# Performance work log

Hardware: AMD Instinct MI355X
Metric: run time of the kernel (lower is better)

Reference implementation:

```python
import jax, jax.numpy as jnp
import numpy as np

N_NODES = 50000
N_REL = 16
D_EMB = 128
D_HID = 128
D_OUT = 128
N_EDGES = 1600000


def _xavier(key, shape, fan_in, fan_out, dtype=jnp.float32):
    lim = float(np.sqrt(6.0 / (fan_in + fan_out)))
    return jax.random.uniform(key, shape, dtype, -lim, lim)


def setup_inputs() -> dict:
    key = jax.random.key(0)
    ks = jax.random.split(key, 10)
    edge_index = jax.random.randint(ks[0], (2, N_EDGES), 0, N_NODES, dtype=jnp.int64)
    edge_type = jax.random.randint(ks[1], (N_EDGES,), 0, N_REL, dtype=jnp.int64)
    emb = _xavier(ks[2], (N_NODES, D_EMB), N_NODES, D_EMB)
    W1 = _xavier(ks[3], (N_REL, D_EMB, D_HID), D_EMB, D_HID)
    root1 = _xavier(ks[4], (D_EMB, D_HID), D_EMB, D_HID)
    b1 = jnp.zeros((D_HID,), jnp.float32)
    W2 = _xavier(ks[5], (N_REL, D_HID, D_OUT), D_HID, D_OUT)
    root2 = _xavier(ks[6], (D_HID, D_OUT), D_HID, D_OUT)
    b2 = jnp.zeros((D_OUT,), jnp.float32)
    return {"edge_index": edge_index, "edge_type": edge_type, "emb": emb,
            "W1": W1, "root1": root1, "b1": b1,
            "W2": W2, "root2": root2, "b2": b2}


def rgcn_conv(x, edge_index, edge_type, W, W_root, b):
    """PyG RGCNConv (num_bases=None): out_i = x_i @ W_root + b + sum_r mean_{j in N_r(i)} x_j @ W_r.
    Mean-aggregate x_j per (dst, relation) first, then apply relation GEMMs (linearity)."""
    src, dst = edge_index[0], edge_index[1]
    seg = dst * N_REL + edge_type                      # [E] composite (node, rel) key
    x_src = x[src]                                     # [E, d] gather
    summed = jax.ops.segment_sum(x_src, seg, num_segments=N_NODES * N_REL)  # [N*R, d]
    cnt = jax.ops.segment_sum(jnp.ones((src.shape[0],), x.dtype), seg,
                              num_segments=N_NODES * N_REL)                 # [N*R]
    agg = summed / jnp.maximum(cnt, 1.0)[:, None]      # mean; empty (i,r) -> 0
    agg = agg.reshape(N_NODES, N_REL, x.shape[1])      # [N, R, d]
    return jnp.einsum('nrd,rdh->nh', agg, W) + x @ W_root + b


def reference(edge_index, edge_type, emb, W1, root1, b1, W2, root2, b2):
    x = emb                                            # embedding.weight: all-node lookup
    x = jax.nn.relu(rgcn_conv(x, edge_index, edge_type, W1, root1, b1))
    # dropout(p=0.5) omitted: eval-mode identity
    x = rgcn_conv(x, edge_index, edge_type, W2, root2, b2)
    return x
```

## Files before the change

kernel.cpp:

```cpp
#include <hip/hip_runtime.h>

#define N_NODES 50000
#define N_REL 16
#define D 128
#define N_SEG (N_NODES * N_REL)
#define N_SEG4 (N_SEG / 4)

typedef short bf16x8 __attribute__((ext_vector_type(8)));
typedef float f32x4 __attribute__((ext_vector_type(4)));
typedef unsigned short u16;
typedef unsigned int u32;

__device__ __forceinline__ u16 f32_to_bf16(float f) {
  u32 u = __builtin_bit_cast(u32, f);
  u32 r = (u + 0x7FFFu + ((u >> 16) & 1u)) >> 16;
  return (u16)r;
}
__device__ __forceinline__ float bf16_to_f32(u16 h) {
  u32 u = ((u32)h) << 16;
  return __builtin_bit_cast(float, u);
}

__global__ __launch_bounds__(256) void k_count(const int* __restrict__ dst,
                                               const int* __restrict__ rel,
                                               int* __restrict__ cnt, int E) {
  int e = (blockIdx.x * blockDim.x + threadIdx.x) * 2;
  if (e < E)     atomicAdd(&cnt[dst[e] * N_REL + rel[e]], 1);
  if (e + 1 < E) atomicAdd(&cnt[dst[e + 1] * N_REL + rel[e + 1]], 1);
}

__global__ __launch_bounds__(256) void k_bsum2(const int4* __restrict__ cnt4,
                                               int* __restrict__ bsum, int n4) {
  __shared__ int sm[256];
  int idx = blockIdx.x * 256 + threadIdx.x;
  int v = 0;
  if (idx < n4) { int4 c = cnt4[idx]; v = c.x + c.y + c.z + c.w; }
  sm[threadIdx.x] = v;
  __syncthreads();
  for (int s = 128; s > 0; s >>= 1) {
    if (threadIdx.x < s) sm[threadIdx.x] += sm[threadIdx.x + s];
    __syncthreads();
  }
  if (threadIdx.x == 0) bsum[blockIdx.x] = sm[0];
}

__global__ __launch_bounds__(1024) void k_bscan2(int* __restrict__ bsum, int nb) {
  __shared__ int sm[1024];
  int i = threadIdx.x;
  int v = (i < nb) ? bsum[i] : 0;
  sm[i] = v;
  __syncthreads();
  for (int s = 1; s < 1024; s <<= 1) {
    int t = (i >= s) ? sm[i - s] : 0;
    __syncthreads();
    sm[i] += t;
    __syncthreads();
  }
  if (i < nb) bsum[i] = sm[i] - v;
}

__global__ __launch_bounds__(256) void k_off2(const int4* __restrict__ cnt4,
                                              const int* __restrict__ bsum,
                                              int* __restrict__ off, int n4) {
  __shared__ int sm[256];
  int idx = blockIdx.x * 256 + threadIdx.x;
  int4 c = {0, 0, 0, 0};
  if (idx < n4) c = cnt4[idx];
  int tsum = c.x + c.y + c.z + c.w;
  sm[threadIdx.x] = tsum;
  __syncthreads();
  for (int s = 1; s < 256; s <<= 1) {
    int t = (threadIdx.x >= s) ? sm[threadIdx.x - s] : 0;
    __syncthreads();
    sm[threadIdx.x] += t;
    __syncthreads();
  }
  int base = bsum[blockIdx.x] + sm[threadIdx.x] - tsum;
  if (idx < n4) {
    int4 o;
    o.x = base;
    o.y = base + c.x;
    o.z = o.y + c.y;
    o.w = o.z + c.z;
    ((int4*)off)[idx] = o;
    if (idx == n4 - 1) off[4 * n4] = o.w + c.w;
  }
}

__global__ __launch_bounds__(256) void k_fill(const int* __restrict__ src,
                                              const int* __restrict__ dst,
                                              const int* __restrict__ rel,
                                              const int* __restrict__ off,
                                              int* __restrict__ cnt,
                                              int* __restrict__ bucket, int E) {
  int e = (blockIdx.x * blockDim.x + threadIdx.x) * 2;
  if (e < E) {
    int seg = dst[e] * N_REL + rel[e];
    int old = atomicSub(&cnt[seg], 1);
    bucket[off[seg] + old - 1] = src[e];
  }
  if (e + 1 < E) {
    int seg = dst[e + 1] * N_REL + rel[e + 1];
    int old = atomicSub(&cnt[seg], 1);
    bucket[off[seg] + old - 1] = src[e + 1];
  }
}

__device__ __forceinline__ void wfrag_one(const float* __restrict__ W,
                                          u16* __restrict__ Wf, int tid) {
  int lane = tid & 63;
  int t = (tid >> 6) & 7;
  int kb = tid >> 9;
  int h = t * 16 + (lane & 15);
  int kbase = kb * 32 + ((lane >> 4) << 3);
  bf16x8 frag;
#pragma unroll
  for (int j = 0; j < 8; ++j) {
    int k = kbase + j;
    frag[j] = (short)f32_to_bf16(W[(size_t)(k >> 7) * (D * D) + (size_t)(k & 127) * D + h]);
  }
  *(bf16x8*)(Wf + (size_t)tid * 8) = frag;
}

#define ZERO_U4 N_SEG4
#define CVT_N4 (N_NODES * D / 4)
#define WF_T (64 * 8 * 64)
#define RF_T (4 * 8 * 64)
#define PREP_TOTAL (ZERO_U4 + CVT_N4 + 2 * WF_T + 2 * RF_T)

__global__ __launch_bounds__(256) void k_prep(int* __restrict__ cnt,
                                              const float* __restrict__ emb,
                                              u16* __restrict__ embb,
                                              const float* __restrict__ W1,
                                              u16* __restrict__ Wf1,
                                              const float* __restrict__ W2,
                                              u16* __restrict__ Wf2,
                                              const float* __restrict__ R1,
                                              u16* __restrict__ Rf1,
                                              const float* __restrict__ R2,
                                              u16* __restrict__ Rf2) {
  int tid = blockIdx.x * blockDim.x + threadIdx.x;
  if (tid < ZERO_U4) {
    uint4 z; z.x = z.y = z.z = z.w = 0u;
    ((uint4*)cnt)[tid] = z;
    return;
  }
  int u = tid - ZERO_U4;
  if (u < CVT_N4) {
    float4 v = ((const float4*)emb)[u];
    u32 p0 = (u32)f32_to_bf16(v.x) | ((u32)f32_to_bf16(v.y) << 16);
    u32 p1 = (u32)f32_to_bf16(v.z) | ((u32)f32_to_bf16(v.w) << 16);
    ((u32*)embb)[u * 2] = p0;
    ((u32*)embb)[u * 2 + 1] = p1;
    return;
  }
  u -= CVT_N4;
  if (u < WF_T) { wfrag_one(W1, Wf1, u); return; }
  u -= WF_T;
  if (u < WF_T) { wfrag_one(W2, Wf2, u); return; }
  u -= WF_T;
  if (u < RF_T) { wfrag_one(R1, Rf1, u); return; }
  u -= RF_T;
  if (u < RF_T) { wfrag_one(R2, Rf2, u); return; }
}

template <int L>
__global__ __launch_bounds__(256) void k_layer(const int* __restrict__ off,
                                               const int* __restrict__ bucket,
                                               const u16* __restrict__ x,
                                               const u16* __restrict__ Wf,
                                               const u16* __restrict__ Rf,
                                               const float* __restrict__ bias,
                                               u16* __restrict__ outb,
                                               float* __restrict__ outf) {
  __shared__ f32x4 red[4][4][64];
  int w = threadIdx.x >> 6;
  int lane = threadIdx.x & 63;
  int node0 = blockIdx.x << 4;
  int m = lane & 15;
  int q = lane >> 4;
  int node = node0 + m;

  f32x4 acc[8];
#pragma unroll
  for (int t = 0; t < 8; ++t)
#pragma unroll
    for (int i = 0; i < 4; ++i) acc[t][i] = 0.0f;

  {
    bf16x8 a = *(const bf16x8*)(x + ((size_t)node << 7) + w * 32 + (q << 3));
    const u16* bp = Rf + ((size_t)w << 12) + ((size_t)lane << 3);
#pragma unroll
    for (int t = 0; t < 8; ++t) {
      bf16x8 b = *(const bf16x8*)(bp + t * 512);
      acc[t] = __builtin_amdgcn_mfma_f32_16x16x32_bf16(a, b, acc[t], 0, 0, 0);
    }
  }

  for (int rr = 0; rr < 4; ++rr) {
    int r = (w << 2) + rr;
    int seg = (node << 4) + r;
    int o0 = off[seg];
    int o1 = off[seg + 1];

    float a0[8], a1[8], a2[8], a3[8];
#pragma unroll
    for (int j = 0; j < 8; ++j) { a0[j] = 0.f; a1[j] = 0.f; a2[j] = 0.f; a3[j] = 0.f; }

    int i = o0;
    int s = (i < o1) ? bucket[i] : 0;
    while (i < o1) {
      const u16* xs = x + ((size_t)s << 7) + (q << 3);
      bf16x8 v0 = *(const bf16x8*)(xs);
      bf16x8 v1 = *(const bf16x8*)(xs + 32);
      bf16x8 v2 = *(const bf16x8*)(xs + 64);
      bf16x8 v3 = *(const bf16x8*)(xs + 96);
      int snext = (i + 1 < o1) ? bucket[i + 1] : 0;
#pragma unroll
      for (int j = 0; j < 8; ++j) {
        a0[j] += bf16_to_f32((u16)v0[j]);
        a1[j] += bf16_to_f32((u16)v1[j]);
        a2[j] += bf16_to_f32((u16)v2[j]);
        a3[j] += bf16_to_f32((u16)v3[j]);
      }
      s = snext;
      ++i;
    }

    float sc = (o1 > o0) ? 1.0f / (float)(o1 - o0) : 0.0f;
    bf16x8 f0, f1, f2, f3;
#pragma unroll
    for (int j = 0; j < 8; ++j) {
      f0[j] = (short)f32_to_bf16(a0[j] * sc);
      f1[j] = (short)f32_to_bf16(a1[j] * sc);
      f2[j] = (short)f32_to_bf16(a2[j] * sc);
      f3[j] = (short)f32_to_bf16(a3[j] * sc);
    }

    const u16* bp = Wf + ((size_t)(r * 4) << 12) + ((size_t)lane << 3);
#pragma unroll
    for (int t = 0; t < 8; ++t) {
      bf16x8 b0 = *(const bf16x8*)(bp + t * 512);
      bf16x8 b1 = *(const bf16x8*)(bp + 4096 + t * 512);
      bf16x8 b2 = *(const bf16x8*)(bp + 8192 + t * 512);
      bf16x8 b3 = *(const bf16x8*)(bp + 12288 + t * 512);
      acc[t] = __builtin_amdgcn_mfma_f32_16x16x32_bf16(f0, b0, acc[t], 0, 0, 0);
      acc[t] = __builtin_amdgcn_mfma_f32_16x16x32_bf16(f1, b1, acc[t], 0, 0, 0);
      acc[t] = __builtin_amdgcn_mfma_f32_16x16x32_bf16(f2, b2, acc[t], 0, 0, 0);
      acc[t] = __builtin_amdgcn_mfma_f32_16x16x32_bf16(f3, b3, acc[t], 0, 0, 0);
    }
  }

#pragma unroll
  for (int half = 0; half < 2; ++half) {
#pragma unroll
    for (int t = 0; t < 4; ++t) red[w][t][lane] = acc[half * 4 + t];
    __syncthreads();
    {
      f32x4 s0 = red[0][w][lane];
      f32x4 s1 = red[1][w][lane];
      f32x4 s2 = red[2][w][lane];
      f32x4 s3 = red[3][w][lane];
      int tt = half * 4 + w;
      int h = tt * 16 + m;
      float bv = bias[h];
#pragma unroll
      for (int r4 = 0; r4 < 4; ++r4) {
        int n = node0 + (q << 2) + r4;
        float v = s0[r4] + s1[r4] + s2[r4] + s3[r4] + bv;
        if (L == 1) {
          v = v > 0.0f ? v : 0.0f;
          outb[(size_t)n * D + h] = f32_to_bf16(v);
        } else {
          outf[(size_t)n * D + h] = v;
        }
      }
    }
    if (half == 0) __syncthreads();
  }
}

extern "C" void kernel_launch(void* const* d_in, const int* in_sizes, int n_in,
                              void* d_out, int out_size, void* d_ws, size_t ws_size,
                              hipStream_t stream) {
  const int* edge_index = (const int*)d_in[0];
  const int* edge_type  = (const int*)d_in[1];
  const float* emb   = (const float*)d_in[2];
  const float* W1    = (const float*)d_in[3];
  const float* root1 = (const float*)d_in[4];
  const float* b1    = (const float*)d_in[5];
  const float* W2    = (const float*)d_in[6];
  const float* root2 = (const float*)d_in[7];
  const float* b2    = (const float*)d_in[8];
  float* out = (float*)d_out;

  int E = in_sizes[0] / 2;
  const int* src = edge_index;
  const int* dst = edge_index + E;
  int scanBlocks = (N_SEG4 + 255) / 256;

  char* ws = (char*)d_ws;
  size_t off_b = 0;
  auto take = [&](size_t bytes) -> char* {
    char* p = ws + off_b;
    off_b += (bytes + 255) & ~(size_t)255;
    return p;
  };
  int*   cnt    = (int*)take((size_t)N_SEG * 4);
  int*   offs   = (int*)take((size_t)(N_SEG + 1) * 4);
  int*   bsum   = (int*)take((size_t)scanBlocks * 4);
  int*   bucket = (int*)take((size_t)E * 4);
  u16*   embb   = (u16*)take((size_t)N_NODES * D * 2);
  u16*   x1     = (u16*)take((size_t)N_NODES * D * 2);
  u16*   Wf1    = (u16*)take((size_t)64 * 8 * 512 * 2);
  u16*   Rf1    = (u16*)take((size_t)4 * 8 * 512 * 2);
  u16*   Wf2    = (u16*)take((size_t)64 * 8 * 512 * 2);
  u16*   Rf2    = (u16*)take((size_t)4 * 8 * 512 * 2);

  int eBlocks2 = ((E + 1) / 2 + 255) / 256;
  int layerBlocks = N_NODES / 16;

  k_prep<<<(PREP_TOTAL + 255) / 256, 256, 0, stream>>>(cnt, emb, embb, W1, Wf1,
                                                       W2, Wf2, root1, Rf1,
                                                       root2, Rf2);

  k_count<<<eBlocks2, 256, 0, stream>>>(dst, edge_type, cnt, E);
  k_bsum2<<<scanBlocks, 256, 0, stream>>>((const int4*)cnt, bsum, N_SEG4);
  k_bscan2<<<1, 1024, 0, stream>>>(bsum, scanBlocks);
  k_off2<<<scanBlocks, 256, 0, stream>>>((const int4*)cnt, bsum, offs, N_SEG4);
  k_fill<<<eBlocks2, 256, 0, stream>>>(src, dst, edge_type, offs, cnt, bucket, E);

  k_layer<1><<<layerBlocks, 256, 0, stream>>>(offs, bucket, embb, Wf1, Rf1, b1,
                                              x1, nullptr);
  k_layer<2><<<layerBlocks, 256, 0, stream>>>(offs, bucket, x1, Wf2, Rf2, b2,
                                              nullptr, out);
}
```

Before: 511.6 us.

## Restructure layer kernel: wave-per-segment-range gather with deep prefetch and LDS staging

```diff
diff --git a/kernel.cpp b/kernel.cpp
--- a/kernel.cpp
+++ b/kernel.cpp
@@ -15,10 +15,6 @@
   u32 u = __builtin_bit_cast(u32, f);
   u32 r = (u + 0x7FFFu + ((u >> 16) & 1u)) >> 16;
   return (u16)r;
-}
-__device__ __forceinline__ float bf16_to_f32(u16 h) {
-  u32 u = ((u32)h) << 16;
-  return __builtin_bit_cast(float, u);
 }
 
 __global__ __launch_bounds__(256) void k_count(const int* __restrict__ dst,
@@ -129,6 +125,7 @@
 #define PREP_TOTAL (ZERO_U4 + CVT_N4 + 2 * WF_T + 2 * RF_T)
 
 __global__ __launch_bounds__(256) void k_prep(int* __restrict__ cnt,
+                                              int* __restrict__ bucket, int E,
                                               const float* __restrict__ emb,
                                               u16* __restrict__ embb,
                                               const float* __restrict__ W1,
@@ -140,6 +137,7 @@
                                               const float* __restrict__ R2,
                                               u16* __restrict__ Rf2) {
   int tid = blockIdx.x * blockDim.x + threadIdx.x;
+  if (tid < 32) bucket[E + tid] = 0;
   if (tid < ZERO_U4) {
     uint4 z; z.x = z.y = z.z = z.w = 0u;
     ((uint4*)cnt)[tid] = z;
@@ -165,7 +163,7 @@
 }
 
 template <int L>
-__global__ __launch_bounds__(256) void k_layer(const int* __restrict__ off,
+__global__ __launch_bounds__(512) void k_layer(const int* __restrict__ off,
                                                const int* __restrict__ bucket,
                                                const u16* __restrict__ x,
                                                const u16* __restrict__ Wf,
@@ -173,110 +171,131 @@
                                                const float* __restrict__ bias,
                                                u16* __restrict__ outb,
                                                float* __restrict__ outf) {
-  __shared__ f32x4 red[4][4][64];
-  int w = threadIdx.x >> 6;
-  int lane = threadIdx.x & 63;
+  __shared__ __align__(16) u32 agg[16 * 16 * 64];
+  __shared__ int offs_sm[257];
+  int tid = threadIdx.x;
+  int w = tid >> 6;
+  int lane = tid & 63;
   int node0 = blockIdx.x << 4;
+
+  if (tid < 257) offs_sm[tid] = off[(node0 << 4) + tid];
+  __syncthreads();
+
+  const u32* xw = (const u32*)x;
+
+  int sbase = w << 5;
+  int W0 = __builtin_amdgcn_readfirstlane(offs_sm[sbase]);
+  int W1 = __builtin_amdgcn_readfirstlane(offs_sm[sbase + 32]);
+  int s = 0;
+  int segstart = W0;
+  int onext = __builtin_amdgcn_readfirstlane(offs_sm[sbase + 1]);
+  float aL = 0.0f, aH = 0.0f;
+
+  auto flushAt = [&](int pos) {
+    while (s < 32 && pos == onext) {
+      int len = onext - segstart;
+      float sc = (len > 0) ? 1.0f / (float)len : 0.0f;
+      u32 p = (u32)f32_to_bf16(aL * sc) | ((u32)f32_to_bf16(aH * sc) << 16);
+      int seg = sbase + s;
+      int mrow = seg >> 4;
+      agg[(seg << 6) + ((((lane >> 2) ^ mrow) << 2) | (lane & 3))] = p;
+      aL = 0.0f; aH = 0.0f;
+      segstart = onext;
+      ++s;
+      onext = (s < 32) ? __builtin_amdgcn_readfirstlane(offs_sm[sbase + s + 1])
+                       : 0x7FFFFFFF;
+    }
+  };
+  flushAt(W0);
+
+  u32 rbuf[8];
+  int ibuf[8];
+#pragma unroll
+  for (int k = 0; k < 8; ++k) {
+    int idx = __builtin_amdgcn_readfirstlane(bucket[W0 + k]);
+    rbuf[k] = xw[((size_t)(u32)idx << 6) + lane];
+    ibuf[k] = __builtin_amdgcn_readfirstlane(bucket[W0 + 8 + k]);
+  }
+
+  int i = W0;
+  while (i + 16 <= W1) {
+#pragma unroll
+    for (int k = 0; k < 8; ++k) {
+      u32 u = rbuf[k];
+      aL += __builtin_bit_cast(float, u << 16);
+      aH += __builtin_bit_cast(float, u & 0xFFFF0000u);
+      flushAt(i + k + 1);
+      rbuf[k] = xw[((size_t)(u32)ibuf[k] << 6) + lane];
+      ibuf[k] = __builtin_amdgcn_readfirstlane(bucket[i + k + 16]);
+    }
+    i += 8;
+  }
+
+  int n = W1 - i;
+#pragma unroll
+  for (int k = 0; k < 8; ++k) {
+    if (k < n) {
+      u32 u = rbuf[k];
+      aL += __builtin_bit_cast(float, u << 16);
+      aH += __builtin_bit_cast(float, u & 0xFFFF0000u);
+      flushAt(i + k + 1);
+    }
+  }
+  u32 r2[8];
+#pragma unroll
+  for (int k = 0; k < 8; ++k)
+    if (8 + k < n) r2[k] = xw[((size_t)(u32)ibuf[k] << 6) + lane];
+#pragma unroll
+  for (int k = 0; k < 8; ++k) {
+    if (8 + k < n) {
+      u32 u = r2[k];
+      aL += __builtin_bit_cast(float, u << 16);
+      aH += __builtin_bit_cast(float, u & 0xFFFF0000u);
+      flushAt(i + 8 + k + 1);
+    }
+  }
+  __syncthreads();
+
+  int q = lane >> 4;
   int m = lane & 15;
-  int q = lane >> 4;
-  int node = node0 + m;
-
-  f32x4 acc[8];
-#pragma unroll
-  for (int t = 0; t < 8; ++t)
-#pragma unroll
-    for (int i = 0; i < 4; ++i) acc[t][i] = 0.0f;
+  const u16* aggh = (const u16*)agg;
+
+  f32x4 acc;
+#pragma unroll
+  for (int j = 0; j < 4; ++j) acc[j] = 0.0f;
 
   {
-    bf16x8 a = *(const bf16x8*)(x + ((size_t)node << 7) + w * 32 + (q << 3));
-    const u16* bp = Rf + ((size_t)w << 12) + ((size_t)lane << 3);
-#pragma unroll
-    for (int t = 0; t < 8; ++t) {
-      bf16x8 b = *(const bf16x8*)(bp + t * 512);
-      acc[t] = __builtin_amdgcn_mfma_f32_16x16x32_bf16(a, b, acc[t], 0, 0, 0);
-    }
-  }
-
-  for (int rr = 0; rr < 4; ++rr) {
-    int r = (w << 2) + rr;
-    int seg = (node << 4) + r;
-    int o0 = off[seg];
-    int o1 = off[seg + 1];
-
-    float a0[8], a1[8], a2[8], a3[8];
-#pragma unroll
-    for (int j = 0; j < 8; ++j) { a0[j] = 0.f; a1[j] = 0.f; a2[j] = 0.f; a3[j] = 0.f; }
-
-    int i = o0;
-    int s = (i < o1) ? bucket[i] : 0;
-    while (i < o1) {
-      const u16* xs = x + ((size_t)s << 7) + (q << 3);
-      bf16x8 v0 = *(const bf16x8*)(xs);
-      bf16x8 v1 = *(const bf16x8*)(xs + 32);
-      bf16x8 v2 = *(const bf16x8*)(xs + 64);
-      bf16x8 v3 = *(const bf16x8*)(xs + 96);
-      int snext = (i + 1 < o1) ? bucket[i + 1] : 0;
-#pragma unroll
-      for (int j = 0; j < 8; ++j) {
-        a0[j] += bf16_to_f32((u16)v0[j]);
-        a1[j] += bf16_to_f32((u16)v1[j]);
-        a2[j] += bf16_to_f32((u16)v2[j]);
-        a3[j] += bf16_to_f32((u16)v3[j]);
-      }
-      s = snext;
-      ++i;
-    }
-
-    float sc = (o1 > o0) ? 1.0f / (float)(o1 - o0) : 0.0f;
-    bf16x8 f0, f1, f2, f3;
-#pragma unroll
-    for (int j = 0; j < 8; ++j) {
-      f0[j] = (short)f32_to_bf16(a0[j] * sc);
-      f1[j] = (short)f32_to_bf16(a1[j] * sc);
-      f2[j] = (short)f32_to_bf16(a2[j] * sc);
-      f3[j] = (short)f32_to_bf16(a3[j] * sc);
-    }
-
-    const u16* bp = Wf + ((size_t)(r * 4) << 12) + ((size_t)lane << 3);
-#pragma unroll
-    for (int t = 0; t < 8; ++t) {
-      bf16x8 b0 = *(const bf16x8*)(bp + t * 512);
-      bf16x8 b1 = *(const bf16x8*)(bp + 4096 + t * 512);
-      bf16x8 b2 = *(const bf16x8*)(bp + 8192 + t * 512);
-      bf16x8 b3 = *(const bf16x8*)(bp + 12288 + t * 512);
-      acc[t] = __builtin_amdgcn_mfma_f32_16x16x32_bf16(f0, b0, acc[t], 0, 0, 0);
-      acc[t] = __builtin_amdgcn_mfma_f32_16x16x32_bf16(f1, b1, acc[t], 0, 0, 0);
-      acc[t] = __builtin_amdgcn_mfma_f32_16x16x32_bf16(f2, b2, acc[t], 0, 0, 0);
-      acc[t] = __builtin_amdgcn_mfma_f32_16x16x32_bf16(f3, b3, acc[t], 0, 0, 0);
-    }
-  }
-
-#pragma unroll
-  for (int half = 0; half < 2; ++half) {
-#pragma unroll
-    for (int t = 0; t < 4; ++t) red[w][t][lane] = acc[half * 4 + t];
-    __syncthreads();
-    {
-      f32x4 s0 = red[0][w][lane];
-      f32x4 s1 = red[1][w][lane];
-      f32x4 s2 = red[2][w][lane];
-      f32x4 s3 = red[3][w][lane];
-      int tt = half * 4 + w;
-      int h = tt * 16 + m;
-      float bv = bias[h];
-#pragma unroll
-      for (int r4 = 0; r4 < 4; ++r4) {
-        int n = node0 + (q << 2) + r4;
-        float v = s0[r4] + s1[r4] + s2[r4] + s3[r4] + bv;
-        if (L == 1) {
-          v = v > 0.0f ? v : 0.0f;
-          outb[(size_t)n * D + h] = f32_to_bf16(v);
-        } else {
-          outf[(size_t)n * D + h] = v;
-        }
-      }
-    }
-    if (half == 0) __syncthreads();
+    const u16* xr = x + ((size_t)(node0 + m) << 7) + (q << 3);
+#pragma unroll
+    for (int kb = 0; kb < 4; ++kb) {
+      bf16x8 a = *(const bf16x8*)(xr + kb * 32);
+      bf16x8 b = *(const bf16x8*)(Rf + ((((kb << 3) + w) << 9) | (lane << 3)));
+      acc = __builtin_amdgcn_mfma_f32_16x16x32_bf16(a, b, acc, 0, 0, 0);
+    }
+  }
+
+  for (int r = 0; r < 16; ++r) {
+#pragma unroll
+    for (int kb = 0; kb < 4; ++kb) {
+      int c = ((kb << 2) | q) ^ m;
+      bf16x8 a = *(const bf16x8*)(aggh + ((((m << 4) | r) << 7) | (c << 3)));
+      bf16x8 b = *(const bf16x8*)(Wf + (((((r << 2) | kb) << 3) + w) << 9) + (lane << 3));
+      acc = __builtin_amdgcn_mfma_f32_16x16x32_bf16(a, b, acc, 0, 0, 0);
+    }
+  }
+
+  int h = (w << 4) + m;
+  float bv = bias[h];
+#pragma unroll
+  for (int j = 0; j < 4; ++j) {
+    int n2 = node0 + (q << 2) + j;
+    float v = acc[j] + bv;
+    if (L == 1) {
+      v = v > 0.0f ? v : 0.0f;
+      outb[(size_t)n2 * D + h] = f32_to_bf16(v);
+    } else {
+      outf[(size_t)n2 * D + h] = v;
+    }
   }
 }
 
@@ -309,7 +328,7 @@
   int*   cnt    = (int*)take((size_t)N_SEG * 4);
   int*   offs   = (int*)take((size_t)(N_SEG + 1) * 4);
   int*   bsum   = (int*)take((size_t)scanBlocks * 4);
-  int*   bucket = (int*)take((size_t)E * 4);
+  int*   bucket = (int*)take((size_t)(E + 32) * 4);
   u16*   embb   = (u16*)take((size_t)N_NODES * D * 2);
   u16*   x1     = (u16*)take((size_t)N_NODES * D * 2);
   u16*   Wf1    = (u16*)take((size_t)64 * 8 * 512 * 2);
@@ -320,9 +339,9 @@
   int eBlocks2 = ((E + 1) / 2 + 255) / 256;
   int layerBlocks = N_NODES / 16;
 
-  k_prep<<<(PREP_TOTAL + 255) / 256, 256, 0, stream>>>(cnt, emb, embb, W1, Wf1,
-                                                       W2, Wf2, root1, Rf1,
-                                                       root2, Rf2);
+  k_prep<<<(PREP_TOTAL + 255) / 256, 256, 0, stream>>>(cnt, bucket, E, emb, embb,
+                                                       W1, Wf1, W2, Wf2,
+                                                       root1, Rf1, root2, Rf2);
 
   k_count<<<eBlocks2, 256, 0, stream>>>(dst, edge_type, cnt, E);
   k_bsum2<<<scanBlocks, 256, 0, stream>>>((const int4*)cnt, bsum, N_SEG4);
@@ -330,8 +349,8 @@
   k_off2<<<scanBlocks, 256, 0, stream>>>((const int4*)cnt, bsum, offs, N_SEG4);
   k_fill<<<eBlocks2, 256, 0, stream>>>(src, dst, edge_type, offs, cnt, bucket, E);
 
-  k_layer<1><<<layerBlocks, 256, 0, stream>>>(offs, bucket, embb, Wf1, Rf1, b1,
+  k_layer<1><<<layerBlocks, 512, 0, stream>>>(offs, bucket, embb, Wf1, Rf1, b1,
                                               x1, nullptr);
-  k_layer<2><<<layerBlocks, 256, 0, stream>>>(offs, bucket, x1, Wf2, Rf2, b2,
+  k_layer<2><<<layerBlocks, 512, 0, stream>>>(offs, bucket, x1, Wf2, Rf2, b2,
                                               nullptr, out);
 }
```

After: 553.0 us. +8.1%, slower.
